# Kernel tuning notes

Measured on AMD Instinct MI355X. Metric: run time of the kernel, lower is better.

## Reference

```python
import jax, jax.numpy as jnp
import numpy as np

NEG_SLOPE = 0.2
EPS = 1e-16
N_NODES, N_EDGES, N_GRAPHS = 50000, 800000, 64
EMB, HID, HEADS = 128, 64, 4


def segment_softmax(scores, seg, num_segments):
    # scores: [E, H], seg: [E] destination ids
    m = jax.ops.segment_max(scores, seg, num_segments=num_segments)
    e = jnp.exp(scores - m[seg])
    s = jax.ops.segment_sum(e, seg, num_segments=num_segments)
    return e / (s[seg] + EPS)


def gat_layer(x, edge_index, W, att_src, att_dst, bias, heads, out_ch, num_nodes):
    # PyG GATConv (add_self_loops handled by caller): linear -> per-edge attn -> segment softmax -> scatter-add
    h = (x @ W).reshape(num_nodes, heads, out_ch)          # [N, H, C]
    a_src = jnp.sum(h * att_src, axis=-1)                  # [N, H]
    a_dst = jnp.sum(h * att_dst, axis=-1)                  # [N, H]
    src, dst = edge_index[0], edge_index[1]
    alpha = jax.nn.leaky_relu(a_src[src] + a_dst[dst], NEG_SLOPE)   # [E, H]
    alpha = segment_softmax(alpha, dst, num_nodes)
    msg = h[src] * alpha[:, :, None]                       # [E, H, C]
    out = jax.ops.segment_sum(msg, dst, num_segments=num_nodes)
    return out.reshape(num_nodes, heads * out_ch) + bias


def setup_inputs() -> dict:
    key = jax.random.key(0)
    ks = jax.random.split(key, 16)
    g = lambda k, shape, fan: jax.random.normal(k, shape, jnp.float32) * (1.0 / np.sqrt(fan))
    x = jax.random.normal(ks[0], (N_NODES, EMB), jnp.float32)
    edge_index = jax.random.randint(ks[1], (2, N_EDGES), 0, N_NODES, dtype=jnp.int64)
    batch_map = jnp.sort(jax.random.randint(ks[2], (N_NODES,), 0, N_GRAPHS, dtype=jnp.int64))
    return {
        'x': x, 'edge_index': edge_index, 'batch_map': batch_map,
        'W1': g(ks[3], (EMB, HEADS * HID), EMB),
        'att_src1': g(ks[4], (HEADS, HID), HID),
        'att_dst1': g(ks[5], (HEADS, HID), HID),
        'b1': jnp.zeros((HEADS * HID,), jnp.float32),
        'W2': g(ks[6], (HEADS * HID, HID), HEADS * HID),
        'att_src2': g(ks[7], (1, HID), HID),
        'att_dst2': g(ks[8], (1, HID), HID),
        'b2': jnp.zeros((HID,), jnp.float32),
        'Wg1': g(ks[9], (HID, HID), HID),
        'bg1': jnp.zeros((HID,), jnp.float32),
        'Wg2': g(ks[10], (HID, 1), HID),
        'bg2': jnp.zeros((1,), jnp.float32),
    }


def reference(x, edge_index, batch_map, W1, att_src1, att_dst1, b1, W2, att_src2, att_dst2, b2, Wg1, bg1, Wg2, bg2):
    n = x.shape[0]
    # GATConv default add_self_loops=True
    loops = jnp.arange(n, dtype=edge_index.dtype)
    ei = jnp.concatenate([edge_index, jnp.stack([loops, loops])], axis=1)
    h = jax.nn.elu(gat_layer(x, ei, W1, att_src1, att_dst1, b1, HEADS, HID, n))
    h = jax.nn.elu(gat_layer(h, ei, W2, att_src2, att_dst2, b2, 1, HID, n))
    # AttentionalAggregation: gate MLP -> segment softmax over graphs -> weighted sum
    gate = jax.nn.relu(h @ Wg1 + bg1) @ Wg2 + bg2          # [N, 1]
    w = segment_softmax(gate, batch_map, N_GRAPHS)         # [N, 1]
    graph_emb = jax.ops.segment_sum(w * h, batch_map, num_segments=N_GRAPHS)
    return graph_emb
```

## Files before the change

kernel.cpp:

```cpp
#include <hip/hip_runtime.h>
#include <math.h>

#define N_NODES 50000
#define N_EDGES 800000
#define E_TOT   850000
#define N_GRAPHS 64
#define EMB 128
#define HID 64
#define HEADS 4
#define NEG_SLOPE 0.2f
#define EPS 1e-16f
#define MAX_DEG 64

typedef short bf16x8 __attribute__((ext_vector_type(8)));
typedef float f32x4  __attribute__((ext_vector_type(4)));

__device__ __forceinline__ float leaky(float x) { return x >= 0.f ? x : NEG_SLOPE * x; }
__device__ __forceinline__ float elu(float x)   { return x > 0.f ? x : expf(x) - 1.f; }

__device__ __forceinline__ unsigned short f2bf(float f) {
    unsigned u = __float_as_uint(f);
    return (unsigned short)((u + 0x7FFFu + ((u >> 16) & 1u)) >> 16);
}
__device__ __forceinline__ float bf2f(unsigned short h) {
    return __uint_as_float((unsigned)h << 16);
}

__device__ __forceinline__ void edge_sd(const int* __restrict__ ei, int e, int& s, int& d) {
    if (e < N_EDGES) { s = ei[e]; d = ei[N_EDGES + e]; }
    else             { s = d = e - N_EDGES; }
}

__device__ __forceinline__ int lbound(const int* __restrict__ a, int n, int v) {
    int lo = 0, hi = n;
    while (lo < hi) { int mid = (lo + hi) >> 1; if (a[mid] < v) lo = mid + 1; else hi = mid; }
    return lo;
}

__global__ void k_zero4(float4* p, int n4) {
    int i = blockIdx.x * blockDim.x + threadIdx.x;
    int stride = gridDim.x * blockDim.x;
    for (; i < n4; i += stride) p[i] = make_float4(0.f, 0.f, 0.f, 0.f);
}

__global__ void k_ell_build(const int* __restrict__ ei, unsigned* __restrict__ cnt,
                            unsigned short* __restrict__ ell) {
    int e = blockIdx.x * blockDim.x + threadIdx.x;
    if (e >= E_TOT) return;
    int s, d; edge_sd(ei, e, s, d);
    unsigned slot = atomicAdd(&cnt[d], 1u);
    if (slot < MAX_DEG) ell[d * MAX_DEG + slot] = (unsigned short)s;
}

__global__ void k_wprep(const float* __restrict__ W1, const float* __restrict__ as1, const float* __restrict__ ad1,
                        const float* __restrict__ W2, const float* __restrict__ as2, const float* __restrict__ ad2,
                        const float* __restrict__ Wg1,
                        unsigned short* __restrict__ W1t, float* __restrict__ v1s, float* __restrict__ v1d,
                        unsigned short* __restrict__ W2t, float* __restrict__ v2s, float* __restrict__ v2d,
                        unsigned short* __restrict__ wg1h, unsigned short* __restrict__ wg1l) {
    int b = blockIdx.x, t = threadIdx.x;
    if (b < 32) {
        for (int i = b * 1024 + t; i < (b + 1) * 1024; i += 256) {
            int c = i >> 7, k = i & 127;
            W1t[i] = f2bf(W1[k * 256 + c]);
        }
    } else if (b < 48) {
        int bb = b - 32;
        for (int i = bb * 1024 + t; i < (bb + 1) * 1024; i += 256) {
            int c = i >> 8, k = i & 255;
            W2t[i] = f2bf(W2[k * 64 + c]);
        }
    } else if (b == 48) {
        for (int i = t; i < 512; i += 256) {
            int h = i >> 7, k = i & 127;
            float s = 0.f, d = 0.f;
            for (int c = 0; c < 64; ++c) {
                float wv = W1[k * 256 + h * 64 + c];
                s = fmaf(wv, as1[h * 64 + c], s);
                d = fmaf(wv, ad1[h * 64 + c], d);
            }
            v1s[i] = s; v1d[i] = d;
        }
    } else if (b == 49) {
        float s = 0.f, d = 0.f;
        for (int cc = 0; cc < 64; ++cc) {
            float wv = W2[t * 64 + cc];
            s = fmaf(wv, as2[cc], s);
            d = fmaf(wv, ad2[cc], d);
        }
        v2s[t] = s; v2d[t] = d;
    } else {
        for (int i = t; i < 4096; i += 256) {
            int c = i >> 6, k = i & 63;
            float v = Wg1[k * 64 + c];
            unsigned short h = f2bf(v);
            wg1h[i] = h;
            wg1l[i] = f2bf(v - bf2f(h));
        }
    }
}

__global__ __launch_bounds__(256)
void k_gemm1_mfma(const float* __restrict__ x, const unsigned short* __restrict__ W1t,
                  const float* __restrict__ v1s, const float* __restrict__ v1d,
                  unsigned short* __restrict__ h1b, float* __restrict__ a_src1,
                  float* __restrict__ a_dst1) {
    int w = threadIdx.x >> 6, l = threadIdx.x & 63;
    int r = l & 15, kg = l >> 4;
    int tile = blockIdx.x;
    const float* xr = x + (size_t)(tile * 16 + r) * 128 + kg * 8;
    bf16x8 af[4];
    float ps = 0.f, pd = 0.f;
    #pragma unroll
    for (int j = 0; j < 4; ++j) {
        float4 f0 = *(const float4*)(xr + j * 32);
        float4 f1 = *(const float4*)(xr + j * 32 + 4);
        const float* vs = v1s + w * 128 + j * 32 + kg * 8;
        const float* vd = v1d + w * 128 + j * 32 + kg * 8;
        float4 s0 = *(const float4*)vs, s1 = *(const float4*)(vs + 4);
        float4 d0 = *(const float4*)vd, d1 = *(const float4*)(vd + 4);
        ps += f0.x*s0.x + f0.y*s0.y + f0.z*s0.z + f0.w*s0.w
            + f1.x*s1.x + f1.y*s1.y + f1.z*s1.z + f1.w*s1.w;
        pd += f0.x*d0.x + f0.y*d0.y + f0.z*d0.z + f0.w*d0.w
            + f1.x*d1.x + f1.y*d1.y + f1.z*d1.z + f1.w*d1.w;
        bf16x8 t;
        t[0] = (short)f2bf(f0.x); t[1] = (short)f2bf(f0.y);
        t[2] = (short)f2bf(f0.z); t[3] = (short)f2bf(f0.w);
        t[4] = (short)f2bf(f1.x); t[5] = (short)f2bf(f1.y);
        t[6] = (short)f2bf(f1.z); t[7] = (short)f2bf(f1.w);
        af[j] = t;
    }
    ps += __shfl_xor(ps, 16); ps += __shfl_xor(ps, 32);
    pd += __shfl_xor(pd, 16); pd += __shfl_xor(pd, 32);
    if (l < 16) {
        a_src1[(size_t)(tile * 16 + r) * 4 + w] = ps;
        a_dst1[(size_t)(tile * 16 + r) * 4 + w] = pd;
    }
    for (int cc = 0; cc < 4; ++cc) {
        int c0 = cc * 64 + w * 16;
        const bf16x8* B = (const bf16x8*)(W1t + (size_t)(c0 + r) * 128 + kg * 8);
        f32x4 acc = {0.f, 0.f, 0.f, 0.f};
        acc = __builtin_amdgcn_mfma_f32_16x16x32_bf16(af[0], B[0],  acc, 0, 0, 0);
        acc = __builtin_amdgcn_mfma_f32_16x16x32_bf16(af[1], B[4],  acc, 0, 0, 0);
        acc = __builtin_amdgcn_mfma_f32_16x16x32_bf16(af[2], B[8],  acc, 0, 0, 0);
        acc = __builtin_amdgcn_mfma_f32_16x16x32_bf16(af[3], B[12], acc, 0, 0, 0);
        #pragma unroll
        for (int j = 0; j < 4; ++j)
            h1b[(size_t)(tile * 16 + kg * 4 + j) * 256 + c0 + r] = f2bf(acc[j]);
    }
}

__global__ __launch_bounds__(1024)
void k_layer1(const unsigned short* __restrict__ ell, const unsigned* __restrict__ cnt,
              const float4* __restrict__ asrc, const float4* __restrict__ adst,
              const unsigned short* __restrict__ h1b, const float4* __restrict__ bias,
              const float4* __restrict__ v2s4, const float4* __restrict__ v2d4,
              const unsigned short* __restrict__ W2t,
              float* __restrict__ a_src2, float* __restrict__ a_dst2,
              unsigned short* __restrict__ h2b) {
    __shared__ float sw[16][MAX_DEG][4];
    __shared__ int   ss[16][MAX_DEG];
    __shared__ unsigned short Ash[16][264];
    int wave = threadIdx.x >> 6, lane = threadIdx.x & 63;
    int node = blockIdx.x * 16 + wave;
    int deg = min((int)cnt[node], MAX_DEG);

    float4 ad = adst[node];
    float a0 = -INFINITY, a1 = -INFINITY, a2 = -INFINITY, a3 = -INFINITY;
    int s = 0;
    if (lane < deg) {
        s = ell[node * MAX_DEG + lane];
        float4 as = asrc[s];
        a0 = leaky(as.x + ad.x); a1 = leaky(as.y + ad.y);
        a2 = leaky(as.z + ad.z); a3 = leaky(as.w + ad.w);
    }
    float m0 = a0, m1 = a1, m2 = a2, m3 = a3;
    for (int o = 32; o > 0; o >>= 1) {
        m0 = fmaxf(m0, __shfl_xor(m0, o)); m1 = fmaxf(m1, __shfl_xor(m1, o));
        m2 = fmaxf(m2, __shfl_xor(m2, o)); m3 = fmaxf(m3, __shfl_xor(m3, o));
    }
    float w0 = lane < deg ? expf(a0 - m0) : 0.f;
    float w1 = lane < deg ? expf(a1 - m1) : 0.f;
    float w2 = lane < deg ? expf(a2 - m2) : 0.f;
    float w3 = lane < deg ? expf(a3 - m3) : 0.f;
    float t0 = w0, t1 = w1, t2 = w2, t3 = w3;
    for (int o = 32; o > 0; o >>= 1) {
        t0 += __shfl_xor(t0, o); t1 += __shfl_xor(t1, o);
        t2 += __shfl_xor(t2, o); t3 += __shfl_xor(t3, o);
    }
    w0 /= (t0 + EPS); w1 /= (t1 + EPS); w2 /= (t2 + EPS); w3 /= (t3 + EPS);
    if (lane < deg) {
        sw[wave][lane][0] = w0; sw[wave][lane][1] = w1;
        sw[wave][lane][2] = w2; sw[wave][lane][3] = w3;
        ss[wave][lane] = s;
    }
    int head = lane >> 4;
    float c0 = 0.f, c1 = 0.f, c2 = 0.f, c3 = 0.f;
    for (int e = 0; e < deg; ++e) {
        int se = ss[wave][e];
        float w = sw[wave][e][head];
        ushort4 h = *(const ushort4*)(h1b + (size_t)se * 256 + lane * 4);
        c0 = fmaf(bf2f(h.x), w, c0); c1 = fmaf(bf2f(h.y), w, c1);
        c2 = fmaf(bf2f(h.z), w, c2); c3 = fmaf(bf2f(h.w), w, c3);
    }
    float4 b = bias[lane];
    float o0 = elu(c0 + b.x), o1 = elu(c1 + b.y), o2 = elu(c2 + b.z), o3 = elu(c3 + b.w);
    *(ushort4*)&Ash[wave][lane * 4] = make_ushort4(f2bf(o0), f2bf(o1), f2bf(o2), f2bf(o3));
    float4 vs = v2s4[lane], vd = v2d4[lane];
    float ps = o0 * vs.x + o1 * vs.y + o2 * vs.z + o3 * vs.w;
    float pd = o0 * vd.x + o1 * vd.y + o2 * vd.z + o3 * vd.w;
    for (int o = 32; o > 0; o >>= 1) { ps += __shfl_xor(ps, o); pd += __shfl_xor(pd, o); }
    if (lane == 0) { a_src2[node] = ps; a_dst2[node] = pd; }

    __syncthreads();
    if (wave < 4) {
        int r = lane & 15, kg = lane >> 4;
        f32x4 acc = {0.f, 0.f, 0.f, 0.f};
        #pragma unroll
        for (int kk = 0; kk < 8; ++kk) {
            bf16x8 afr = *(const bf16x8*)&Ash[r][kg * 8 + kk * 32];
            bf16x8 bfr = *(const bf16x8*)(W2t + (size_t)(wave * 16 + r) * 256 + kg * 8 + kk * 32);
            acc = __builtin_amdgcn_mfma_f32_16x16x32_bf16(afr, bfr, acc, 0, 0, 0);
        }
        #pragma unroll
        for (int j = 0; j < 4; ++j)
            h2b[(size_t)(blockIdx.x * 16 + kg * 4 + j) * 64 + wave * 16 + r] = f2bf(acc[j]);
    }
}

__global__ __launch_bounds__(1024)
void k_layer2(const unsigned short* __restrict__ ell, const unsigned* __restrict__ cnt,
              const float* __restrict__ asrc, const float* __restrict__ adst,
              const unsigned short* __restrict__ h2b, const float* __restrict__ bias,
              const unsigned short* __restrict__ wg1h, const unsigned short* __restrict__ wg1l,
              const float* __restrict__ bg1, const float* __restrict__ Wg2,
              const float* __restrict__ bg2,
              float* __restrict__ out2, float* __restrict__ gate) {
    __shared__ float sw[16][MAX_DEG];
    __shared__ int   ss[16][MAX_DEG];
    __shared__ unsigned short Ah[16][72], Al[16][72];
    __shared__ float gp[4][16];
    int wave = threadIdx.x >> 6, lane = threadIdx.x & 63;
    int half = lane >> 5, li = lane & 31;
    int node = blockIdx.x * 16 + wave;
    int deg = min((int)cnt[node], MAX_DEG);

    float adv = adst[node];
    float a = -INFINITY;
    int s = 0;
    if (lane < deg) {
        s = ell[node * MAX_DEG + lane];
        a = leaky(asrc[s] + adv);
    }
    float m = a;
    for (int o = 32; o > 0; o >>= 1) m = fmaxf(m, __shfl_xor(m, o));
    float w = lane < deg ? expf(a - m) : 0.f;
    float t = w;
    for (int o = 32; o > 0; o >>= 1) t += __shfl_xor(t, o);
    w /= (t + EPS);
    if (lane < deg) { sw[wave][lane] = w; ss[wave][lane] = s; }

    float c0 = 0.f, c1 = 0.f;
    for (int e = 0; e < deg; e += 2) {
        int row = e + half;
        if (row < deg) {
            int se = ss[wave][row];
            float ww = sw[wave][row];
            unsigned u = *(const unsigned*)(h2b + (size_t)se * 64 + li * 2);
            c0 = fmaf(__uint_as_float(u << 16), ww, c0);
            c1 = fmaf(__uint_as_float(u & 0xffff0000u), ww, c1);
        }
    }
    c0 += __shfl_xor(c0, 32);
    c1 += __shfl_xor(c1, 32);
    if (half == 0) {
        float o0 = elu(c0 + bias[li * 2]);
        float o1 = elu(c1 + bias[li * 2 + 1]);
        *(float2*)(out2 + (size_t)node * 64 + li * 2) = make_float2(o0, o1);
        unsigned short h0 = f2bf(o0), h1 = f2bf(o1);
        *(unsigned*)&Ah[wave][li * 2] = ((unsigned)h1 << 16) | h0;
        unsigned short l0 = f2bf(o0 - bf2f(h0)), l1 = f2bf(o1 - bf2f(h1));
        *(unsigned*)&Al[wave][li * 2] = ((unsigned)l1 << 16) | l0;
    }

    __syncthreads();
    if (wave < 4) {
        int r = lane & 15, kg = lane >> 4;
        const bf16x8* Bh = (const bf16x8*)(wg1h + (size_t)(wave * 16 + r) * 64 + kg * 8);
        const bf16x8* Bl = (const bf16x8*)(wg1l + (size_t)(wave * 16 + r) * 64 + kg * 8);
        bf16x8 ah0 = *(const bf16x8*)&Ah[r][kg * 8];
        bf16x8 ah1 = *(const bf16x8*)&Ah[r][kg * 8 + 32];
        bf16x8 al0 = *(const bf16x8*)&Al[r][kg * 8];
        bf16x8 al1 = *(const bf16x8*)&Al[r][kg * 8 + 32];
        f32x4 acc = {0.f, 0.f, 0.f, 0.f};
        acc = __builtin_amdgcn_mfma_f32_16x16x32_bf16(ah0, Bh[0], acc, 0, 0, 0);
        acc = __builtin_amdgcn_mfma_f32_16x16x32_bf16(ah1, Bh[4], acc, 0, 0, 0);
        acc = __builtin_amdgcn_mfma_f32_16x16x32_bf16(ah0, Bl[0], acc, 0, 0, 0);
        acc = __builtin_amdgcn_mfma_f32_16x16x32_bf16(ah1, Bl[4], acc, 0, 0, 0);
        acc = __builtin_amdgcn_mfma_f32_16x16x32_bf16(al0, Bh[0], acc, 0, 0, 0);
        acc = __builtin_amdgcn_mfma_f32_16x16x32_bf16(al1, Bh[4], acc, 0, 0, 0);
        int col = wave * 16 + r;
        float wg2 = Wg2[col], bb = bg1[col];
        float part[4];
        #pragma unroll
        for (int j = 0; j < 4; ++j) part[j] = fmaxf(acc[j] + bb, 0.f) * wg2;
        #pragma unroll
        for (int o = 8; o > 0; o >>= 1) {
            #pragma unroll
            for (int j = 0; j < 4; ++j) part[j] += __shfl_xor(part[j], o);
        }
        if (r == 0) {
            #pragma unroll
            for (int j = 0; j < 4; ++j) gp[wave][kg * 4 + j] = part[j];
        }
    }
    __syncthreads();
    if (threadIdx.x < 16)
        gate[blockIdx.x * 16 + threadIdx.x] = gp[0][threadIdx.x] + gp[1][threadIdx.x]
                                            + gp[2][threadIdx.x] + gp[3][threadIdx.x] + bg2[0];
}

__global__ __launch_bounds__(1024)
void k_final(const float* __restrict__ gate, const float* __restrict__ hfin,
             const int* __restrict__ batch, float* __restrict__ out) {
    __shared__ float red[16];
    __shared__ float redc[16][64];
    int g = blockIdx.x;
    int lo = lbound(batch, N_NODES, g);
    int hi = lbound(batch, N_NODES, g + 1);
    int tid = threadIdx.x, wave = tid >> 6, lane = tid & 63;

    float m = -INFINITY;
    for (int i = lo + tid; i < hi; i += 1024) m = fmaxf(m, gate[i]);
    for (int o = 32; o > 0; o >>= 1) m = fmaxf(m, __shfl_xor(m, o));
    if (lane == 0) red[wave] = m;
    __syncthreads();
    m = -INFINITY;
    #pragma unroll
    for (int i = 0; i < 16; ++i) m = fmaxf(m, red[i]);
    __syncthreads();

    float s = 0.f;
    for (int i = lo + tid; i < hi; i += 1024) s += expf(gate[i] - m);
    for (int o = 32; o > 0; o >>= 1) s += __shfl_xor(s, o);
    if (lane == 0) red[wave] = s;
    __syncthreads();
    s = 0.f;
    #pragma unroll
    for (int i = 0; i < 16; ++i) s += red[i];

    float acc = 0.f;
    for (int i = lo + wave; i < hi; i += 16)
        acc = fmaf(expf(gate[i] - m), hfin[(size_t)i * 64 + lane], acc);
    redc[wave][lane] = acc;
    __syncthreads();
    if (tid < 64) {
        float r = 0.f;
        #pragma unroll
        for (int i = 0; i < 16; ++i) r += redc[i][tid];
        out[g * 64 + tid] = r / (s + EPS);
    }
}

extern "C" void kernel_launch(void* const* d_in, const int* in_sizes, int n_in,
                              void* d_out, int out_size, void* d_ws, size_t ws_size,
                              hipStream_t stream) {
    const float* x    = (const float*)d_in[0];
    const int*   ei   = (const int*)d_in[1];
    const int*   batch= (const int*)d_in[2];
    const float* W1   = (const float*)d_in[3];
    const float* as1  = (const float*)d_in[4];
    const float* ad1  = (const float*)d_in[5];
    const float* b1   = (const float*)d_in[6];
    const float* W2   = (const float*)d_in[7];
    const float* as2  = (const float*)d_in[8];
    const float* ad2  = (const float*)d_in[9];
    const float* b2   = (const float*)d_in[10];
    const float* Wg1  = (const float*)d_in[11];
    const float* bg1  = (const float*)d_in[12];
    const float* Wg2  = (const float*)d_in[13];
    const float* bg2  = (const float*)d_in[14];
    float* out = (float*)d_out;

    char* W = (char*)d_ws;
    size_t off = 0;
    unsigned* cnt = (unsigned*)(W + off); off += (size_t)N_NODES * 4;
    size_t zero_bytes = off;
    unsigned short* ell  = (unsigned short*)(W + off); off += (size_t)N_NODES * MAX_DEG * 2;
    unsigned short* h1b  = (unsigned short*)(W + off); size_t h1_off = off;
    off += (size_t)N_NODES * 256 * 2;
    float* a_src1 = (float*)(W + off); off += (size_t)N_NODES * HEADS * 4;
    float* a_dst1 = (float*)(W + off); off += (size_t)N_NODES * HEADS * 4;
    float* a_src2 = (float*)(W + off); off += (size_t)N_NODES * 4;
    float* a_dst2 = (float*)(W + off); off += (size_t)N_NODES * 4;
    float* out2   = (float*)(W + off); off += (size_t)N_NODES * HID * 4;
    float* gate   = (float*)(W + off); off += (size_t)N_NODES * 4;
    unsigned short* W1t = (unsigned short*)(W + off); off += (size_t)128 * 256 * 2;
    float* v1s = (float*)(W + off); off += 512 * 4;
    float* v1d = (float*)(W + off); off += 512 * 4;
    unsigned short* W2t = (unsigned short*)(W + off); off += (size_t)64 * 256 * 2;
    float* v2s = (float*)(W + off); off += 256 * 4;
    float* v2d = (float*)(W + off); off += 256 * 4;
    unsigned short* wg1h = (unsigned short*)(W + off); off += (size_t)64 * 64 * 2;
    unsigned short* wg1l = (unsigned short*)(W + off); off += (size_t)64 * 64 * 2;
    unsigned short* h2b = (unsigned short*)(W + off); off += (size_t)N_NODES * HID * 2;
    (void)h1_off; (void)ws_size; (void)in_sizes; (void)n_in; (void)out_size;

    k_zero4<<<64, 256, 0, stream>>>((float4*)W, (int)(zero_bytes / 16));
    k_ell_build<<<(E_TOT + 255) / 256, 256, 0, stream>>>(ei, cnt, ell);
    k_wprep<<<51, 256, 0, stream>>>(W1, as1, ad1, W2, as2, ad2, Wg1,
                                    W1t, v1s, v1d, W2t, v2s, v2d, wg1h, wg1l);

    k_gemm1_mfma<<<N_NODES / 16, 256, 0, stream>>>(x, W1t, v1s, v1d, h1b, a_src1, a_dst1);
    k_layer1<<<N_NODES / 16, 1024, 0, stream>>>(ell, cnt, (const float4*)a_src1,
        (const float4*)a_dst1, h1b, (const float4*)b1,
        (const float4*)v2s, (const float4*)v2d, W2t, a_src2, a_dst2, h2b);
    k_layer2<<<N_NODES / 16, 1024, 0, stream>>>(ell, cnt, a_src2, a_dst2, h2b, b2,
                                                wg1h, wg1l, bg1, Wg2, bg2, out2, gate);
    k_final<<<N_GRAPHS, 1024, 0, stream>>>(gate, out2, batch, out);
}
```

Measured before the change: 285.5 us.

## Split layer-1 into attention, column-sliced gather, and separate GEMM2 kernels

The fused layer-1 kernel is replaced by three kernels. One computes the softmax weights and packs them, with the source index, into per-head arrays. One gathers neighbour features from a new channel-plane layout of h1 (8 planes of 32 columns), so each block's working set is one slice, which aims to improve L2/cache locality for the random gathers. The last runs GEMM2 as its own kernel. The cost is extra global traffic for the packed weights (about 51MB written and read), out1b, the partial attention sums, and two more launches.

Measured after the change: 378.3 us. 32.5% more time.

```diff
diff --git a/kernel.cpp b/kernel.cpp
--- a/kernel.cpp
+++ b/kernel.cpp
@@ -103,7 +103,7 @@
 __global__ __launch_bounds__(256)
 void k_gemm1_mfma(const float* __restrict__ x, const unsigned short* __restrict__ W1t,
                   const float* __restrict__ v1s, const float* __restrict__ v1d,
-                  unsigned short* __restrict__ h1b, float* __restrict__ a_src1,
+                  unsigned short* __restrict__ h1p, float* __restrict__ a_src1,
                   float* __restrict__ a_dst1) {
     int w = threadIdx.x >> 6, l = threadIdx.x & 63;
     int r = l & 15, kg = l >> 4;
@@ -144,25 +144,22 @@
         acc = __builtin_amdgcn_mfma_f32_16x16x32_bf16(af[1], B[4],  acc, 0, 0, 0);
         acc = __builtin_amdgcn_mfma_f32_16x16x32_bf16(af[2], B[8],  acc, 0, 0, 0);
         acc = __builtin_amdgcn_mfma_f32_16x16x32_bf16(af[3], B[12], acc, 0, 0, 0);
+        int c = c0 + r;
+        int plane = c >> 5, within = c & 31;
         #pragma unroll
-        for (int j = 0; j < 4; ++j)
-            h1b[(size_t)(tile * 16 + kg * 4 + j) * 256 + c0 + r] = f2bf(acc[j]);
-    }
-}
-
-__global__ __launch_bounds__(1024)
-void k_layer1(const unsigned short* __restrict__ ell, const unsigned* __restrict__ cnt,
-              const float4* __restrict__ asrc, const float4* __restrict__ adst,
-              const unsigned short* __restrict__ h1b, const float4* __restrict__ bias,
-              const float4* __restrict__ v2s4, const float4* __restrict__ v2d4,
-              const unsigned short* __restrict__ W2t,
-              float* __restrict__ a_src2, float* __restrict__ a_dst2,
-              unsigned short* __restrict__ h2b) {
-    __shared__ float sw[16][MAX_DEG][4];
-    __shared__ int   ss[16][MAX_DEG];
-    __shared__ unsigned short Ash[16][264];
+        for (int j = 0; j < 4; ++j) {
+            int nr = tile * 16 + kg * 4 + j;
+            h1p[((size_t)plane * N_NODES + nr) * 32 + within] = f2bf(acc[j]);
+        }
+    }
+}
+
+__global__ __launch_bounds__(256)
+void k_attn1(const unsigned short* __restrict__ ell, const unsigned* __restrict__ cnt,
+             const float4* __restrict__ asrc, const float4* __restrict__ adst,
+             unsigned* __restrict__ wele) {
     int wave = threadIdx.x >> 6, lane = threadIdx.x & 63;
-    int node = blockIdx.x * 16 + wave;
+    int node = blockIdx.x * 4 + wave;
     int deg = min((int)cnt[node], MAX_DEG);
 
     float4 ad = adst[node];
@@ -190,41 +187,93 @@
     }
     w0 /= (t0 + EPS); w1 /= (t1 + EPS); w2 /= (t2 + EPS); w3 /= (t3 + EPS);
     if (lane < deg) {
-        sw[wave][lane][0] = w0; sw[wave][lane][1] = w1;
-        sw[wave][lane][2] = w2; sw[wave][lane][3] = w3;
-        ss[wave][lane] = s;
-    }
-    int head = lane >> 4;
-    float c0 = 0.f, c1 = 0.f, c2 = 0.f, c3 = 0.f;
-    for (int e = 0; e < deg; ++e) {
-        int se = ss[wave][e];
-        float w = sw[wave][e][head];
-        ushort4 h = *(const ushort4*)(h1b + (size_t)se * 256 + lane * 4);
-        c0 = fmaf(bf2f(h.x), w, c0); c1 = fmaf(bf2f(h.y), w, c1);
-        c2 = fmaf(bf2f(h.z), w, c2); c3 = fmaf(bf2f(h.w), w, c3);
-    }
-    float4 b = bias[lane];
-    float o0 = elu(c0 + b.x), o1 = elu(c1 + b.y), o2 = elu(c2 + b.z), o3 = elu(c3 + b.w);
-    *(ushort4*)&Ash[wave][lane * 4] = make_ushort4(f2bf(o0), f2bf(o1), f2bf(o2), f2bf(o3));
-    float4 vs = v2s4[lane], vd = v2d4[lane];
-    float ps = o0 * vs.x + o1 * vs.y + o2 * vs.z + o3 * vs.w;
-    float pd = o0 * vd.x + o1 * vd.y + o2 * vd.z + o3 * vd.w;
-    for (int o = 32; o > 0; o >>= 1) { ps += __shfl_xor(ps, o); pd += __shfl_xor(pd, o); }
-    if (lane == 0) { a_src2[node] = ps; a_dst2[node] = pd; }
-
-    __syncthreads();
-    if (wave < 4) {
-        int r = lane & 15, kg = lane >> 4;
-        f32x4 acc = {0.f, 0.f, 0.f, 0.f};
+        unsigned hi = (unsigned)s << 16;
+        size_t base = (size_t)node * 64 + lane;
+        wele[base]                            = hi | f2bf(w0);
+        wele[(size_t)N_NODES * 64 + base]     = hi | f2bf(w1);
+        wele[(size_t)N_NODES * 64 * 2 + base] = hi | f2bf(w2);
+        wele[(size_t)N_NODES * 64 * 3 + base] = hi | f2bf(w3);
+    }
+}
+
+__global__ __launch_bounds__(256)
+void k_gather1(const unsigned* __restrict__ wele, const unsigned* __restrict__ cnt,
+               const unsigned short* __restrict__ h1p, const float* __restrict__ bias,
+               const float* __restrict__ v2s, const float* __restrict__ v2d,
+               unsigned short* __restrict__ out1b,
+               float* __restrict__ p2s, float* __restrict__ p2d) {
+    int b = blockIdx.x;
+    int slice = b & 7, tile = b >> 3;
+    int wave = threadIdx.x >> 6, lane = threadIdx.x & 63;
+    int head = slice >> 1;
+    const unsigned* wp = wele + (size_t)head * N_NODES * 64;
+    const unsigned short* hp = h1p + (size_t)slice * N_NODES * 32;
+    int cbase = slice * 32 + (lane & 7) * 4;
+    float4 bb = *(const float4*)(bias + cbase);
+    float4 vs = *(const float4*)(v2s + cbase);
+    float4 vd = *(const float4*)(v2d + cbase);
+    #pragma unroll
+    for (int j = 0; j < 4; ++j) {
+        int node = tile * 16 + wave * 4 + j;
+        int deg = min((int)cnt[node], MAX_DEG);
+        unsigned entry = lane < deg ? wp[(size_t)node * 64 + lane] : 0u;
+        float a0 = 0.f, a1 = 0.f, a2 = 0.f, a3 = 0.f;
+        for (int e0 = 0; e0 < deg; e0 += 8) {
+            int row = e0 + (lane >> 3);
+            unsigned ue = __shfl(entry, row);
+            if (row < deg) {
+                int s = ue >> 16;
+                float w = bf2f((unsigned short)(ue & 0xffffu));
+                ushort4 h = *(const ushort4*)(hp + (size_t)s * 32 + (lane & 7) * 4);
+                a0 = fmaf(bf2f(h.x), w, a0); a1 = fmaf(bf2f(h.y), w, a1);
+                a2 = fmaf(bf2f(h.z), w, a2); a3 = fmaf(bf2f(h.w), w, a3);
+            }
+        }
+        a0 += __shfl_xor(a0, 8); a0 += __shfl_xor(a0, 16); a0 += __shfl_xor(a0, 32);
+        a1 += __shfl_xor(a1, 8); a1 += __shfl_xor(a1, 16); a1 += __shfl_xor(a1, 32);
+        a2 += __shfl_xor(a2, 8); a2 += __shfl_xor(a2, 16); a2 += __shfl_xor(a2, 32);
+        a3 += __shfl_xor(a3, 8); a3 += __shfl_xor(a3, 16); a3 += __shfl_xor(a3, 32);
+        float o0 = elu(a0 + bb.x), o1 = elu(a1 + bb.y), o2 = elu(a2 + bb.z), o3 = elu(a3 + bb.w);
+        float ps = o0 * vs.x + o1 * vs.y + o2 * vs.z + o3 * vs.w;
+        float pd = o0 * vd.x + o1 * vd.y + o2 * vd.z + o3 * vd.w;
+        ps += __shfl_xor(ps, 1); ps += __shfl_xor(ps, 2); ps += __shfl_xor(ps, 4);
+        pd += __shfl_xor(pd, 1); pd += __shfl_xor(pd, 2); pd += __shfl_xor(pd, 4);
+        if (lane < 8)
+            *(ushort4*)(out1b + (size_t)node * 256 + cbase) =
+                make_ushort4(f2bf(o0), f2bf(o1), f2bf(o2), f2bf(o3));
+        if (lane == 0) {
+            p2s[(size_t)node * 8 + slice] = ps;
+            p2d[(size_t)node * 8 + slice] = pd;
+        }
+    }
+}
+
+__global__ __launch_bounds__(256)
+void k_gemm2_mfma(const unsigned short* __restrict__ amat, const unsigned short* __restrict__ W2t,
+                  const float* __restrict__ p2s, const float* __restrict__ p2d,
+                  unsigned short* __restrict__ h2b, float* __restrict__ a_src2,
+                  float* __restrict__ a_dst2) {
+    int w = threadIdx.x >> 6, l = threadIdx.x & 63;
+    int r = l & 15, kg = l >> 4;
+    int tile = blockIdx.x;
+    const bf16x8* A = (const bf16x8*)(amat + (size_t)(tile * 16 + r) * 256 + kg * 8);
+    const bf16x8* B = (const bf16x8*)(W2t + (size_t)(w * 16 + r) * 256 + kg * 8);
+    f32x4 acc = {0.f, 0.f, 0.f, 0.f};
+    #pragma unroll
+    for (int kk = 0; kk < 8; ++kk)
+        acc = __builtin_amdgcn_mfma_f32_16x16x32_bf16(A[kk * 4], B[kk * 4], acc, 0, 0, 0);
+    #pragma unroll
+    for (int j = 0; j < 4; ++j)
+        h2b[(size_t)(tile * 16 + kg * 4 + j) * 64 + w * 16 + r] = f2bf(acc[j]);
+    if (w == 0 && l < 16) {
+        int node = tile * 16 + l;
+        float s = 0.f, d = 0.f;
         #pragma unroll
-        for (int kk = 0; kk < 8; ++kk) {
-            bf16x8 afr = *(const bf16x8*)&Ash[r][kg * 8 + kk * 32];
-            bf16x8 bfr = *(const bf16x8*)(W2t + (size_t)(wave * 16 + r) * 256 + kg * 8 + kk * 32);
-            acc = __builtin_amdgcn_mfma_f32_16x16x32_bf16(afr, bfr, acc, 0, 0, 0);
-        }
-        #pragma unroll
-        for (int j = 0; j < 4; ++j)
-            h2b[(size_t)(blockIdx.x * 16 + kg * 4 + j) * 64 + wave * 16 + r] = f2bf(acc[j]);
+        for (int j = 0; j < 8; ++j) {
+            s += p2s[(size_t)node * 8 + j];
+            d += p2d[(size_t)node * 8 + j];
+        }
+        a_src2[node] = s; a_dst2[node] = d;
     }
 }
 
@@ -387,13 +436,14 @@
     unsigned* cnt = (unsigned*)(W + off); off += (size_t)N_NODES * 4;
     size_t zero_bytes = off;
     unsigned short* ell  = (unsigned short*)(W + off); off += (size_t)N_NODES * MAX_DEG * 2;
-    unsigned short* h1b  = (unsigned short*)(W + off); size_t h1_off = off;
+    unsigned short* h1p  = (unsigned short*)(W + off); size_t h1_off = off;
     off += (size_t)N_NODES * 256 * 2;
     float* a_src1 = (float*)(W + off); off += (size_t)N_NODES * HEADS * 4;
     float* a_dst1 = (float*)(W + off); off += (size_t)N_NODES * HEADS * 4;
-    float* a_src2 = (float*)(W + off); off += (size_t)N_NODES * 4;
-    float* a_dst2 = (float*)(W + off); off += (size_t)N_NODES * 4;
-    float* out2   = (float*)(W + off); off += (size_t)N_NODES * HID * 4;
+    unsigned* wele = (unsigned*)(W + off); off += (size_t)HEADS * N_NODES * MAX_DEG * 4;
+    unsigned short* out1b = (unsigned short*)(W + off); off += (size_t)N_NODES * 256 * 2;
+    float* p2s = (float*)(W + off); off += (size_t)N_NODES * 8 * 4;
+    float* p2d = (float*)(W + off); off += (size_t)N_NODES * 8 * 4;
     float* gate   = (float*)(W + off); off += (size_t)N_NODES * 4;
     unsigned short* W1t = (unsigned short*)(W + off); off += (size_t)128 * 256 * 2;
     float* v1s = (float*)(W + off); off += 512 * 4;
@@ -403,18 +453,25 @@
     float* v2d = (float*)(W + off); off += 256 * 4;
     unsigned short* wg1h = (unsigned short*)(W + off); off += (size_t)64 * 64 * 2;
     unsigned short* wg1l = (unsigned short*)(W + off); off += (size_t)64 * 64 * 2;
-    unsigned short* h2b = (unsigned short*)(W + off); off += (size_t)N_NODES * HID * 2;
-    (void)h1_off; (void)ws_size; (void)in_sizes; (void)n_in; (void)out_size;
+    size_t aoff = h1_off;
+    unsigned short* h2b = (unsigned short*)(W + aoff); aoff += (size_t)N_NODES * HID * 2;
+    float* out2   = (float*)(W + aoff); aoff += (size_t)N_NODES * HID * 4;
+    float* a_src2 = (float*)(W + aoff); aoff += (size_t)N_NODES * 4;
+    float* a_dst2 = (float*)(W + aoff); aoff += (size_t)N_NODES * 4;
+    (void)ws_size; (void)in_sizes; (void)n_in; (void)out_size;
 
     k_zero4<<<64, 256, 0, stream>>>((float4*)W, (int)(zero_bytes / 16));
     k_ell_build<<<(E_TOT + 255) / 256, 256, 0, stream>>>(ei, cnt, ell);
     k_wprep<<<51, 256, 0, stream>>>(W1, as1, ad1, W2, as2, ad2, Wg1,
                                     W1t, v1s, v1d, W2t, v2s, v2d, wg1h, wg1l);
 
-    k_gemm1_mfma<<<N_NODES / 16, 256, 0, stream>>>(x, W1t, v1s, v1d, h1b, a_src1, a_dst1);
-    k_layer1<<<N_NODES / 16, 1024, 0, stream>>>(ell, cnt, (const float4*)a_src1,
-        (const float4*)a_dst1, h1b, (const float4*)b1,
-        (const float4*)v2s, (const float4*)v2d, W2t, a_src2, a_dst2, h2b);
+    k_gemm1_mfma<<<N_NODES / 16, 256, 0, stream>>>(x, W1t, v1s, v1d, h1p, a_src1, a_dst1);
+    k_attn1<<<N_NODES / 4, 256, 0, stream>>>(ell, cnt, (const float4*)a_src1,
+                                             (const float4*)a_dst1, wele);
+    k_gather1<<<(N_NODES / 16) * 8, 256, 0, stream>>>(wele, cnt, h1p, b1, v2s, v2d,
+                                                      out1b, p2s, p2d);
+
+    k_gemm2_mfma<<<N_NODES / 16, 256, 0, stream>>>(out1b, W2t, p2s, p2d, h2b, a_src2, a_dst2);
     k_layer2<<<N_NODES / 16, 1024, 0, stream>>>(ell, cnt, a_src2, a_dst2, h2b, b2,
                                                 wg1h, wg1l, bg1, Wg2, bg2, out2, gate);
     k_final<<<N_GRAPHS, 1024, 0, stream>>>(gate, out2, batch, out);
```
